# Performance work log

Measured on AMD Instinct MI355X. Metric: run time of the kernel, lower is better.

## Reference

```python
import jax, jax.numpy as jnp
import numpy as np

B, D_MODEL, N, H = 4, 256, 2048, 4
HEAD_DIM = D_MODEL // H  # 64


def _rotate_half(x):
    # x: [..., d] with d even; pairs (x1, x2) -> (-x2, x1)
    x = x.reshape(x.shape[:-1] + (x.shape[-1] // 2, 2))
    x1, x2 = x[..., 0], x[..., 1]
    return jnp.stack((-x2, x1), axis=-1).reshape(x.shape[:-2] + (-1,))


def _apply_rope(freqs, t):
    # freqs: [2, n, d] (cos, sin); t: [b, h, n, d]
    return t * freqs[0] + _rotate_half(t) * freqs[1]


def setup_inputs() -> dict:
    key = jax.random.key(0)
    ks = jax.random.split(key, 12)
    s = 0.02
    inp = {
        "query": jax.random.normal(ks[0], (B, D_MODEL, N), jnp.float32),
        "key": jax.random.normal(ks[1], (B, D_MODEL, N), jnp.float32),
        "value": jax.random.normal(ks[2], (B, D_MODEL, N), jnp.float32),
        "encoding": jax.random.normal(ks[3], (2, N, HEAD_DIM), jnp.float32),
        "Wq": jax.random.normal(ks[4], (D_MODEL, D_MODEL), jnp.float32) * s,
        "bq": jnp.zeros((D_MODEL,), jnp.float32),
        "Wk": jax.random.normal(ks[5], (D_MODEL, D_MODEL), jnp.float32) * s,
        "bk": jnp.zeros((D_MODEL,), jnp.float32),
        "Wv": jax.random.normal(ks[6], (D_MODEL, D_MODEL), jnp.float32) * s,
        "bv": jnp.zeros((D_MODEL,), jnp.float32),
        "Wm": jax.random.normal(ks[7], (D_MODEL, D_MODEL), jnp.float32) * s,
        "bm": jnp.zeros((D_MODEL,), jnp.float32),
    }
    return inp


def _proj(W, b, x):
    # 1x1 Conv1d == channel matmul: x [b, c_in, n] -> [b, c_out, n]
    return jnp.einsum('oi,bin->bon', W, x) + b[None, :, None]


def reference(query, key, value, encoding, Wq, bq, Wk, bk, Wv, bv, Wm, bm):
    b = query.shape[0]
    # project and split channels into (head_dim, heads): [b, d, h, n]
    q = _proj(Wq, bq, query).reshape(b, HEAD_DIM, H, -1)
    k = _proj(Wk, bk, key).reshape(b, HEAD_DIM, H, -1)
    v = _proj(Wv, bv, value).reshape(b, HEAD_DIM, H, -1)
    # RoPE on [b, h, n, d] layout
    q = jnp.transpose(_apply_rope(encoding, jnp.transpose(q, (0, 2, 3, 1))), (0, 3, 1, 2))
    k = jnp.transpose(_apply_rope(encoding, jnp.transpose(k, (0, 2, 3, 1))), (0, 3, 1, 2))
    # attention: scores [b, h, n, m]
    scores = jnp.einsum('bdhn,bdhm->bhnm', q, k) / jnp.sqrt(jnp.float32(HEAD_DIM))
    prob = jax.nn.softmax(scores, axis=-1)
    x = jnp.einsum('bhnm,bdhm->bdhn', prob, v)
    x = x.reshape(b, HEAD_DIM * H, -1)
    return _proj(Wm, bm, x)
```

## Files before the change

kernel.cpp:

```cpp
#include <hip/hip_runtime.h>
#include <stdint.h>

#define NSEQ 2048

typedef __attribute__((ext_vector_type(4))) float f32x4;
typedef __attribute__((ext_vector_type(8))) short s16x8;
typedef _Float16 f16x8 __attribute__((ext_vector_type(8)));

#define OFF_XT  0u
#define OFF_W   12582912u
#define OFF_QR  13107200u
#define OFF_KR  17301504u
#define OFF_VT  21495808u
#define OFF_XA  0u

__device__ __forceinline__ short f2h(float f) {
  _Float16 h = (_Float16)f;
  return __builtin_bit_cast(short, h);
}
__device__ __forceinline__ int swz64(int row, int slot) {
  return row * 64 + ((slot ^ ((row >> 1) & 3)) << 4);
}
__device__ __forceinline__ int swz128(int row, int slot) {
  return row * 128 + ((slot ^ (row & 7)) << 4);
}
#define MFMA(a, b, c) __builtin_amdgcn_mfma_f32_16x16x32_f16(a, b, c, 0, 0, 0)

__global__ void k_convw(const float* __restrict__ Wq, const float* __restrict__ Wk,
                        const float* __restrict__ Wv, const float* __restrict__ Wm,
                        char* __restrict__ ws) {
  int o = blockIdx.x, which = blockIdx.y, i = threadIdx.x;
  const float* src = which == 0 ? Wq : which == 1 ? Wk : which == 2 ? Wv : Wm;
  short* dst = (short*)(ws + OFF_W) + which * 65536;
  float val = (which < 3) ? src[o * 256 + i] : src[o * 256 + ((i & 63) << 2) + (i >> 6)];
  dst[o * 256 + i] = f2h(val);
}

__global__ __launch_bounds__(256) void k_trans(const float* __restrict__ q,
    const float* __restrict__ k, const float* __restrict__ v, char* __restrict__ ws) {
  int tensor = blockIdx.z >> 2, b = blockIdx.z & 3;
  const float* src = tensor == 0 ? q : (tensor == 1 ? k : v);
  short* dst = (short*)(ws + OFF_XT) + (tensor * 4 + b) * 524288;
  int n0 = blockIdx.x * 64, i0 = blockIdx.y * 64;
  __shared__ float tile[64][65];
  int t = threadIdx.x;
  int nl = t & 63, ib = (t >> 6) * 16;
#pragma unroll
  for (int r = 0; r < 16; ++r)
    tile[ib + r][nl] = src[(b * 256 + i0 + ib + r) * 2048 + n0 + nl];
  __syncthreads();
  int nr = t >> 2, ic = (t & 3) * 16;
  short tmp[16];
#pragma unroll
  for (int j = 0; j < 16; ++j) tmp[j] = f2h(tile[ic + j][nr]);
  short* dp = &dst[(n0 + nr) * 256 + i0 + ic];
  *(s16x8*)dp = *(const s16x8*)&tmp[0];
  *(s16x8*)(dp + 8) = *(const s16x8*)&tmp[8];
}

__device__ __forceinline__ void gemm128(const short* __restrict__ W, const short* __restrict__ X,
                                        int o0, int n0, short* As, short* Bs, f32x4 acc[4][4]) {
  int t = threadIdx.x;
  int lane = t & 63, g = lane >> 4, c = lane & 15, wave = t >> 6;
  int wo = (wave >> 1) * 64, wn = (wave & 1) * 64;
  int row = t >> 2, slot = t & 3;
  for (int kk = 0; kk < 8; ++kk) {
    __syncthreads();
    int koff = kk * 32 + slot * 8;
    *(s16x8*)((char*)As + swz64(row, slot))      = *(const s16x8*)&W[(o0 + row) * 256 + koff];
    *(s16x8*)((char*)As + swz64(row + 64, slot)) = *(const s16x8*)&W[(o0 + row + 64) * 256 + koff];
    *(s16x8*)((char*)Bs + swz64(row, slot))      = *(const s16x8*)&X[(n0 + row) * 256 + koff];
    *(s16x8*)((char*)Bs + swz64(row + 64, slot)) = *(const s16x8*)&X[(n0 + row + 64) * 256 + koff];
    __syncthreads();
    f16x8 af[4], bfr[4];
#pragma unroll
    for (int f = 0; f < 4; ++f) {
      af[f]  = *(const f16x8*)((char*)As + swz64(wo + f * 16 + c, g));
      bfr[f] = *(const f16x8*)((char*)Bs + swz64(wn + f * 16 + c, g));
    }
#pragma unroll
    for (int i = 0; i < 4; ++i)
#pragma unroll
      for (int j = 0; j < 4; ++j)
        acc[i][j] = MFMA(af[i], bfr[j], acc[i][j]);
  }
}

__global__ __launch_bounds__(256) void k_proj(const float* __restrict__ enc,
    const float* __restrict__ bq, const float* __restrict__ bk, const float* __restrict__ bv,
    char* __restrict__ ws) {
  int proj = blockIdx.z >> 2, b = blockIdx.z & 3;
  const short* W = (const short*)(ws + OFF_W) + proj * 65536;
  const short* X = (const short*)(ws + OFF_XT) + (proj * 4 + b) * 524288;
  int o0 = blockIdx.y * 128, n0 = blockIdx.x * 128;
  __shared__ short As[128 * 32], Bs[128 * 32];
  f32x4 acc[4][4] = {};
  gemm128(W, X, o0, n0, As, Bs, acc);
  int t = threadIdx.x, lane = t & 63, g = lane >> 4, c = lane & 15, wave = t >> 6;
  int wo = (wave >> 1) * 64, wn = (wave & 1) * 64;
  const float* bias = proj == 0 ? bq : (proj == 1 ? bk : bv);
  if (proj < 2) {
    short* dst = (short*)(ws + (proj == 0 ? OFF_QR : OFF_KR));
    float scale = proj == 0 ? 0.125f : 1.0f;
    float sgn = (g & 1) ? 1.0f : -1.0f;
#pragma unroll
    for (int i = 0; i < 4; ++i) {
      int ob = o0 + wo + i * 16 + g * 4;
      int d = ob >> 2;
#pragma unroll
      for (int j = 0; j < 4; ++j) {
        int n = n0 + wn + j * 16 + c;
        float cv = enc[n * 64 + d], sv = enc[131072 + n * 64 + d];
#pragma unroll
        for (int r = 0; r < 4; ++r) {
          float val = acc[i][j][r] + bias[ob + r];
          float par = __shfl_xor(val, 16, 64);
          float res = (val * cv + sgn * par * sv) * scale;
          dst[((b * 4 + r) * 2048 + n) * 64 + d] = f2h(res);
        }
      }
    }
  } else {
    short* dst = (short*)(ws + OFF_VT);
#pragma unroll
    for (int i = 0; i < 4; ++i) {
      int ob = o0 + wo + i * 16 + g * 4;
      int d = ob >> 2;
#pragma unroll
      for (int j = 0; j < 4; ++j) {
        int n = n0 + wn + j * 16 + c;
#pragma unroll
        for (int r = 0; r < 4; ++r) {
          float val = acc[i][j][r] + bias[ob + r];
          dst[((b * 4 + r) * 64 + d) * 2048 + n] = f2h(val);
        }
      }
    }
  }
}

__global__ __launch_bounds__(256) void k_attn(char* __restrict__ ws) {
  int bh = blockIdx.y;
  int t = threadIdx.x, wave = t >> 6, lane = t & 63, g = lane >> 4, c = lane & 15;
  int nw = blockIdx.x * 64 + wave * 16;
  const short* Q = (const short*)(ws + OFF_QR) + bh * 131072;
  const short* K = (const short*)(ws + OFF_KR) + bh * 131072;
  const short* V = (const short*)(ws + OFF_VT) + bh * 131072;
  short* XA = (short*)(ws + OFF_XA);
  __shared__ short Ks[64 * 64], Vs[64 * 64], Ps[4][16 * 64];
  char* Pb = (char*)Ps[wave];
  f16x8 qf0 = *(const f16x8*)&Q[(nw + c) * 64 + g * 8];
  f16x8 qf1 = *(const f16x8*)&Q[(nw + c) * 64 + 32 + g * 8];
  f32x4 po[4] = {};
  float mrun[4], lrun[4];
#pragma unroll
  for (int r = 0; r < 4; ++r) { mrun[r] = -1e30f; lrun[r] = 0.f; }
  int sr = t >> 3, sl = t & 7;
  for (int m0 = 0; m0 < 2048; m0 += 64) {
    __syncthreads();
    *(s16x8*)((char*)Ks + swz128(sr, sl))      = *(const s16x8*)&K[(m0 + sr) * 64 + sl * 8];
    *(s16x8*)((char*)Ks + swz128(sr + 32, sl)) = *(const s16x8*)&K[(m0 + sr + 32) * 64 + sl * 8];
    *(s16x8*)((char*)Vs + swz128(sr, sl))      = *(const s16x8*)&V[sr * 2048 + m0 + sl * 8];
    *(s16x8*)((char*)Vs + swz128(sr + 32, sl)) = *(const s16x8*)&V[(sr + 32) * 2048 + m0 + sl * 8];
    __syncthreads();
    f32x4 s[4] = {};
#pragma unroll
    for (int fj = 0; fj < 4; ++fj) {
      f16x8 k0 = *(const f16x8*)((char*)Ks + swz128(fj * 16 + c, g));
      f16x8 k1 = *(const f16x8*)((char*)Ks + swz128(fj * 16 + c, 4 + g));
      s[fj] = MFMA(qf0, k0, s[fj]);
      s[fj] = MFMA(qf1, k1, s[fj]);
    }
    float pm[4], nm[4], corr[4], rs[4];
#pragma unroll
    for (int r = 0; r < 4; ++r) {
      pm[r] = fmaxf(fmaxf(s[0][r], s[1][r]), fmaxf(s[2][r], s[3][r]));
#pragma unroll
      for (int d_ = 1; d_ < 16; d_ <<= 1) pm[r] = fmaxf(pm[r], __shfl_xor(pm[r], d_, 64));
      nm[r] = fmaxf(mrun[r], pm[r]);
      corr[r] = __expf(mrun[r] - nm[r]);
      mrun[r] = nm[r];
      rs[r] = 0.f;
    }
    float p[4][4];
#pragma unroll
    for (int fj = 0; fj < 4; ++fj)
#pragma unroll
      for (int r = 0; r < 4; ++r) {
        p[fj][r] = __expf(s[fj][r] - nm[r]);
        rs[r] += p[fj][r];
      }
#pragma unroll
    for (int r = 0; r < 4; ++r) {
#pragma unroll
      for (int d_ = 1; d_ < 16; d_ <<= 1) rs[r] += __shfl_xor(rs[r], d_, 64);
      lrun[r] = lrun[r] * corr[r] + rs[r];
    }
#pragma unroll
    for (int fd = 0; fd < 4; ++fd)
#pragma unroll
      for (int r = 0; r < 4; ++r) po[fd][r] *= corr[r];
#pragma unroll
    for (int fj = 0; fj < 4; ++fj)
#pragma unroll
      for (int r = 0; r < 4; ++r) {
        int rr = g * 4 + r, mm = fj * 16 + c;
        *(short*)(Pb + swz128(rr, mm >> 3) + (mm & 7) * 2) = f2h(p[fj][r]);
      }
    asm volatile("s_waitcnt lgkmcnt(0)" ::: "memory");
    f16x8 pa0 = *(const f16x8*)(Pb + swz128(c, g));
    f16x8 pa1 = *(const f16x8*)(Pb + swz128(c, 4 + g));
#pragma unroll
    for (int fd = 0; fd < 4; ++fd) {
      int dd = fd * 16 + c;
      f16x8 vb0 = *(const f16x8*)((char*)Vs + swz128(dd, g));
      f16x8 vb1 = *(const f16x8*)((char*)Vs + swz128(dd, 4 + g));
      po[fd] = MFMA(pa0, vb0, po[fd]);
      po[fd] = MFMA(pa1, vb1, po[fd]);
    }
  }
  int b = bh >> 2, h = bh & 3;
#pragma unroll
  for (int fd = 0; fd < 4; ++fd) {
    int d = fd * 16 + c;
#pragma unroll
    for (int r = 0; r < 4; ++r) {
      int n = nw + g * 4 + r;
      float val = po[fd][r] / lrun[r];
      XA[(b * 2048 + n) * 256 + h * 64 + d] = f2h(val);
    }
  }
}

__global__ __launch_bounds__(256) void k_final(const float* __restrict__ bm,
    float* __restrict__ out, char* __restrict__ ws) {
  int b = blockIdx.z;
  const short* W = (const short*)(ws + OFF_W) + 3 * 65536;
  const short* X = (const short*)(ws + OFF_XA) + b * 524288;
  int o0 = blockIdx.y * 128, n0 = blockIdx.x * 128;
  __shared__ short As[128 * 32], Bs[128 * 32];
  f32x4 acc[4][4] = {};
  gemm128(W, X, o0, n0, As, Bs, acc);
  int t = threadIdx.x, lane = t & 63, g = lane >> 4, c = lane & 15, wave = t >> 6;
  int wo = (wave >> 1) * 64, wn = (wave & 1) * 64;
#pragma unroll
  for (int i = 0; i < 4; ++i) {
    int ob = o0 + wo + i * 16 + g * 4;
#pragma unroll
    for (int j = 0; j < 4; ++j) {
      int n = n0 + wn + j * 16 + c;
#pragma unroll
      for (int r = 0; r < 4; ++r)
        out[(b * 256 + ob + r) * 2048 + n] = acc[i][j][r] + bm[ob + r];
    }
  }
}

extern "C" void kernel_launch(void* const* d_in, const int* in_sizes, int n_in,
                              void* d_out, int out_size, void* d_ws, size_t ws_size,
                              hipStream_t stream) {
  (void)in_sizes; (void)n_in; (void)out_size; (void)ws_size;
  const float* q   = (const float*)d_in[0];
  const float* k   = (const float*)d_in[1];
  const float* v   = (const float*)d_in[2];
  const float* enc = (const float*)d_in[3];
  const float* Wq  = (const float*)d_in[4];
  const float* bq  = (const float*)d_in[5];
  const float* Wk  = (const float*)d_in[6];
  const float* bk  = (const float*)d_in[7];
  const float* Wv  = (const float*)d_in[8];
  const float* bv  = (const float*)d_in[9];
  const float* Wm  = (const float*)d_in[10];
  const float* bm  = (const float*)d_in[11];
  char* ws = (char*)d_ws;
  float* out = (float*)d_out;
  hipLaunchKernelGGL(k_convw, dim3(256, 4), dim3(256), 0, stream, Wq, Wk, Wv, Wm, ws);
  hipLaunchKernelGGL(k_trans, dim3(32, 4, 12), dim3(256), 0, stream, q, k, v, ws);
  hipLaunchKernelGGL(k_proj, dim3(16, 2, 12), dim3(256), 0, stream, enc, bq, bk, bv, ws);
  hipLaunchKernelGGL(k_attn, dim3(32, 16), dim3(256), 0, stream, ws);
  hipLaunchKernelGGL(k_final, dim3(16, 2, 4), dim3(256), 0, stream, bm, out, ws);
}
```

Measured before the change: 186.2 us.

## Split attention along key dimension with combine kernel and register-prefetched K/V

Splits the key sequence into two halves, doubling the attention grid to 1024 blocks, and writes partial outputs plus row max and sum to workspace. A new combine kernel merges them with log-sum-exp weights. The K/V tile loads are prefetched into registers one tile ahead, and s_setprio and sched_barrier hints are placed around the MFMA sections. This targets low occupancy from only 512 blocks on a 256-CU part and exposed global load latency. In exchange it adds an extra kernel launch, extra workspace traffic and fp16 rounding of the partial outputs.

```diff
diff --git a/kernel.cpp b/kernel.cpp
--- a/kernel.cpp
+++ b/kernel.cpp
@@ -8,15 +8,21 @@
 typedef _Float16 f16x8 __attribute__((ext_vector_type(8)));
 
 #define OFF_XT  0u
+#define OFF_XA  0u
+#define OFF_PO  4194304u
 #define OFF_W   12582912u
 #define OFF_QR  13107200u
 #define OFF_KR  17301504u
 #define OFF_VT  21495808u
-#define OFF_XA  0u
+#define OFF_M   25690112u
+#define OFF_L   25952256u
 
 __device__ __forceinline__ short f2h(float f) {
   _Float16 h = (_Float16)f;
   return __builtin_bit_cast(short, h);
+}
+__device__ __forceinline__ float h2f(short s) {
+  return (float)__builtin_bit_cast(_Float16, s);
 }
 __device__ __forceinline__ int swz64(int row, int slot) {
   return row * 64 + ((slot ^ ((row >> 1) & 3)) << 4);
@@ -139,14 +145,13 @@
   }
 }
 
-__global__ __launch_bounds__(256) void k_attn(char* __restrict__ ws) {
-  int bh = blockIdx.y;
+__global__ __launch_bounds__(256, 4) void k_attn(char* __restrict__ ws) {
+  int bh = blockIdx.y, ms = blockIdx.z;
   int t = threadIdx.x, wave = t >> 6, lane = t & 63, g = lane >> 4, c = lane & 15;
   int nw = blockIdx.x * 64 + wave * 16;
   const short* Q = (const short*)(ws + OFF_QR) + bh * 131072;
   const short* K = (const short*)(ws + OFF_KR) + bh * 131072;
   const short* V = (const short*)(ws + OFF_VT) + bh * 131072;
-  short* XA = (short*)(ws + OFF_XA);
   __shared__ short Ks[64 * 64], Vs[64 * 64], Ps[4][16 * 64];
   char* Pb = (char*)Ps[wave];
   f16x8 qf0 = *(const f16x8*)&Q[(nw + c) * 64 + g * 8];
@@ -156,14 +161,24 @@
 #pragma unroll
   for (int r = 0; r < 4; ++r) { mrun[r] = -1e30f; lrun[r] = 0.f; }
   int sr = t >> 3, sl = t & 7;
-  for (int m0 = 0; m0 < 2048; m0 += 64) {
-    __syncthreads();
-    *(s16x8*)((char*)Ks + swz128(sr, sl))      = *(const s16x8*)&K[(m0 + sr) * 64 + sl * 8];
-    *(s16x8*)((char*)Ks + swz128(sr + 32, sl)) = *(const s16x8*)&K[(m0 + sr + 32) * 64 + sl * 8];
-    *(s16x8*)((char*)Vs + swz128(sr, sl))      = *(const s16x8*)&V[sr * 2048 + m0 + sl * 8];
-    *(s16x8*)((char*)Vs + swz128(sr + 32, sl)) = *(const s16x8*)&V[(sr + 32) * 2048 + m0 + sl * 8];
-    __syncthreads();
+  const int mb = ms * 1024;
+
+  s16x8 rk0, rk1, rv0, rv1, sk0, sk1, sv0, sv1;
+  auto LD = [&](int m0, s16x8& a, s16x8& b2, s16x8& c2, s16x8& d2) {
+    a  = *(const s16x8*)&K[(m0 + sr) * 64 + sl * 8];
+    b2 = *(const s16x8*)&K[(m0 + sr + 32) * 64 + sl * 8];
+    c2 = *(const s16x8*)&V[sr * 2048 + m0 + sl * 8];
+    d2 = *(const s16x8*)&V[(sr + 32) * 2048 + m0 + sl * 8];
+  };
+  auto ST = [&](const s16x8& a, const s16x8& b2, const s16x8& c2, const s16x8& d2) {
+    *(s16x8*)((char*)Ks + swz128(sr, sl))      = a;
+    *(s16x8*)((char*)Ks + swz128(sr + 32, sl)) = b2;
+    *(s16x8*)((char*)Vs + swz128(sr, sl))      = c2;
+    *(s16x8*)((char*)Vs + swz128(sr + 32, sl)) = d2;
+  };
+  auto COMPUTE = [&]() {
     f32x4 s[4] = {};
+    __builtin_amdgcn_s_setprio(1);
 #pragma unroll
     for (int fj = 0; fj < 4; ++fj) {
       f16x8 k0 = *(const f16x8*)((char*)Ks + swz128(fj * 16 + c, g));
@@ -171,6 +186,7 @@
       s[fj] = MFMA(qf0, k0, s[fj]);
       s[fj] = MFMA(qf1, k1, s[fj]);
     }
+    __builtin_amdgcn_s_setprio(0);
     float pm[4], nm[4], corr[4], rs[4];
 #pragma unroll
     for (int r = 0; r < 4; ++r) {
@@ -208,8 +224,10 @@
         *(short*)(Pb + swz128(rr, mm >> 3) + (mm & 7) * 2) = f2h(p[fj][r]);
       }
     asm volatile("s_waitcnt lgkmcnt(0)" ::: "memory");
+    __builtin_amdgcn_sched_barrier(0);
     f16x8 pa0 = *(const f16x8*)(Pb + swz128(c, g));
     f16x8 pa1 = *(const f16x8*)(Pb + swz128(c, 4 + g));
+    __builtin_amdgcn_s_setprio(1);
 #pragma unroll
     for (int fd = 0; fd < 4; ++fd) {
       int dd = fd * 16 + c;
@@ -218,18 +236,68 @@
       po[fd] = MFMA(pa0, vb0, po[fd]);
       po[fd] = MFMA(pa1, vb1, po[fd]);
     }
-  }
-  int b = bh >> 2, h = bh & 3;
+    __builtin_amdgcn_s_setprio(0);
+  };
+
+  LD(mb, rk0, rk1, rv0, rv1);
+  for (int tt = 0; tt < 16; tt += 2) {
+    __syncthreads();
+    ST(rk0, rk1, rv0, rv1);
+    LD(mb + (tt + 1) * 64, sk0, sk1, sv0, sv1);
+    __syncthreads();
+    COMPUTE();
+    __syncthreads();
+    ST(sk0, sk1, sv0, sv1);
+    if (tt + 2 < 16) LD(mb + (tt + 2) * 64, rk0, rk1, rv0, rv1);
+    __syncthreads();
+    COMPUTE();
+  }
+
+  short* PO = (short*)(ws + OFF_PO);
+  float* Mm = (float*)(ws + OFF_M);
+  float* Ll = (float*)(ws + OFF_L);
+  int base = (ms * 16 + bh) * 2048;
 #pragma unroll
   for (int fd = 0; fd < 4; ++fd) {
     int d = fd * 16 + c;
 #pragma unroll
     for (int r = 0; r < 4; ++r) {
       int n = nw + g * 4 + r;
-      float val = po[fd][r] / lrun[r];
-      XA[(b * 2048 + n) * 256 + h * 64 + d] = f2h(val);
-    }
-  }
+      PO[(base + n) * 64 + d] = f2h(po[fd][r] / lrun[r]);
+    }
+  }
+  if (c == 0) {
+#pragma unroll
+    for (int r = 0; r < 4; ++r) {
+      int n = nw + g * 4 + r;
+      Mm[base + n] = mrun[r];
+      Ll[base + n] = lrun[r];
+    }
+  }
+}
+
+__global__ __launch_bounds__(256) void k_comb(char* __restrict__ ws) {
+  int t = threadIdx.x;
+  int row = blockIdx.x * 32 + (t >> 3);
+  int bh = row >> 11, n = row & 2047;
+  int dc = (t & 7) * 8;
+  const short* PO = (const short*)(ws + OFF_PO);
+  const float* Mm = (const float*)(ws + OFF_M);
+  const float* Ll = (const float*)(ws + OFF_L);
+  float m1 = Mm[row], m2 = Mm[32768 + row];
+  float l1 = Ll[row], l2 = Ll[32768 + row];
+  float M = fmaxf(m1, m2);
+  float w1 = l1 * __expf(m1 - M), w2 = l2 * __expf(m2 - M);
+  float inv = 1.f / (w1 + w2);
+  float a1 = w1 * inv, a2 = w2 * inv;
+  s16x8 o1 = *(const s16x8*)&PO[row * 64 + dc];
+  s16x8 o2 = *(const s16x8*)&PO[(32768 + row) * 64 + dc];
+  short res[8];
+#pragma unroll
+  for (int j = 0; j < 8; ++j) res[j] = f2h(a1 * h2f(o1[j]) + a2 * h2f(o2[j]));
+  short* XA = (short*)(ws + OFF_XA);
+  int b = bh >> 2, h = bh & 3;
+  *(s16x8*)&XA[(b * 2048 + n) * 256 + h * 64 + dc] = *(const s16x8*)res;
 }
 
 __global__ __launch_bounds__(256) void k_final(const float* __restrict__ bm,
@@ -277,6 +345,7 @@
   hipLaunchKernelGGL(k_convw, dim3(256, 4), dim3(256), 0, stream, Wq, Wk, Wv, Wm, ws);
   hipLaunchKernelGGL(k_trans, dim3(32, 4, 12), dim3(256), 0, stream, q, k, v, ws);
   hipLaunchKernelGGL(k_proj, dim3(16, 2, 12), dim3(256), 0, stream, enc, bq, bk, bv, ws);
-  hipLaunchKernelGGL(k_attn, dim3(32, 16), dim3(256), 0, stream, ws);
+  hipLaunchKernelGGL(k_attn, dim3(32, 16, 2), dim3(256), 0, stream, ws);
+  hipLaunchKernelGGL(k_comb, dim3(1024), dim3(256), 0, stream, ws);
   hipLaunchKernelGGL(k_final, dim3(16, 2, 4), dim3(256), 0, stream, bm, out, ws);
 }
```

Result: faster. 182.5 us (-2.0%).
